# Kernel tuning notes

Measured on AMD Instinct MI355X. Metric: run time of the kernel, lower is better.

## Reference

```python
import jax, jax.numpy as jnp
import numpy as np

B, T, D, F, E, K = 2, 2048, 1024, 4096, 8, 2

def setup_inputs() -> dict:
    key = jax.random.key(0)
    k0, k1, k2, k3 = jax.random.split(key, 4)
    return {
        "x": jax.random.normal(k0, (B, T, D), jnp.float32),
        "Wg": jax.random.normal(k1, (D, E), jnp.float32) * (D ** -0.5),
        "W1": jax.random.normal(k2, (E, D, F), jnp.float32) * (D ** -0.5),
        "b1": jnp.zeros((E, F), jnp.float32),
        "W2": jax.random.normal(k3, (E, F, D), jnp.float32) * (F ** -0.5),
        "b2": jnp.zeros((E, D), jnp.float32),
        "topk": K,
    }

def reference(x, Wg, W1, b1, W2, b2, topk):
    n_experts = Wg.shape[-1]
    # Gating logits [B, T, E]
    gating = jnp.einsum('btd,de->bte', x, Wg)
    _, idx = jax.lax.top_k(gating, topk)
    # 0/1 mask of selected experts per token [B, T, E]
    mask = jax.nn.one_hot(idx, n_experts, dtype=x.dtype).sum(axis=-2)
    # Source does `gating -= 1/mask - 1`: no-op where mask==1, -inf where mask==0
    gate = jax.nn.softmax(jnp.where(mask > 0, gating, -jnp.inf), axis=-1)
    # Dense masked per-expert compute, exactly as the source (expert(x * mask_e))
    xm = x[:, :, None, :] * mask[:, :, :, None]          # [B, T, E, D]
    h = jax.nn.gelu(jnp.einsum('bted,edf->btef', xm, W1) + b1)  # [B, T, E, F]
    out_e = jnp.einsum('btef,efd->bted', h, W2) + b2     # [B, T, E, D]
    # Gate and sum over experts
    return jnp.sum(out_e * gate[..., None], axis=-2)      # [B, T, D]
```

## Files before the change

### kernel.cpp

```cpp
#include <hip/hip_runtime.h>
#include <hip/hip_bf16.h>
#include <math.h>

#define NB 2
#define NT 2048
#define NTOK 4096
#define DD 1024
#define FF 4096
#define NE 8
#define KSEL 2
#define BM 128
#define BN 128
#define BK 32
#define ROWCAP 9216
#define ROWTILES 72
#define KP2 2

typedef __attribute__((ext_vector_type(8))) short short8_t;
typedef __attribute__((ext_vector_type(4))) float f32x4;

__device__ __forceinline__ unsigned short f2bf(float f){
  unsigned u = __float_as_uint(f);
  unsigned r = (u + 0x7fffu + ((u >> 16) & 1u)) >> 16;
  return (unsigned short)r;
}

__device__ __forceinline__ int xcd_swz(int lin, int nwg){
  int q = nwg >> 3, r = nwg & 7;
  int xcd = lin & 7, idx = lin >> 3;
  return (xcd < r ? xcd * (q + 1) : r * (q + 1) + (xcd - r) * q) + idx;
}

#define GLOAD_LDS(g, l) \
  __builtin_amdgcn_global_load_lds((const __attribute__((address_space(1))) void*)(g), \
                                   (__attribute__((address_space(3))) void*)(l), 16, 0, 0)
#define VMCNT0 asm volatile("s_waitcnt vmcnt(0)" ::: "memory")
#define RAWBAR __builtin_amdgcn_s_barrier()


__global__ void k_prep(const float* __restrict__ x, const float* __restrict__ wg,
                       short* __restrict__ xb, int* __restrict__ topk_idx,
                       float* __restrict__ topk_gate, int* __restrict__ counts){
  int wid = threadIdx.x >> 6, lane = threadIdx.x & 63;
  int t = blockIdx.x * 4 + wid;
  const float* xr = x + (size_t)t * DD;
  short* xbr = xb + (size_t)t * DD;
  double acc[NE];
#pragma unroll
  for (int e = 0; e < NE; ++e) acc[e] = 0.0;
#pragma unroll
  for (int p = 0; p < 4; ++p){
    int d = p * 256 + lane * 4;
    float4 v = *(const float4*)(xr + d);
    short4 o;
    o.x = (short)f2bf(v.x); o.y = (short)f2bf(v.y);
    o.z = (short)f2bf(v.z); o.w = (short)f2bf(v.w);
    *(short4*)(xbr + d) = o;
    const float* w0 = wg + (size_t)d * NE;
    float vv[4] = {v.x, v.y, v.z, v.w};
#pragma unroll
    for (int j = 0; j < 4; ++j){
      double xv = (double)vv[j];
#pragma unroll
      for (int e = 0; e < NE; ++e) acc[e] += xv * (double)w0[j * NE + e];
    }
  }
#pragma unroll
  for (int e = 0; e < NE; ++e){
#pragma unroll
    for (int s = 32; s; s >>= 1) acc[e] += __shfl_xor(acc[e], s, 64);
  }
  if (lane == 0){
    int i0 = 0; double v0 = acc[0];
#pragma unroll
    for (int e = 1; e < NE; ++e) if (acc[e] > v0){ v0 = acc[e]; i0 = e; }
    int i1 = -1; double v1 = -1e300;
#pragma unroll
    for (int e = 0; e < NE; ++e) if (e != i0 && acc[e] > v1){ v1 = acc[e]; i1 = e; }
    double g0 = 1.0 / (1.0 + exp(v1 - v0));
    topk_idx[2 * t] = i0; topk_idx[2 * t + 1] = i1;
    topk_gate[2 * t] = (float)g0; topk_gate[2 * t + 1] = (float)(1.0 - g0);
    atomicAdd(&counts[i0], 1);
    atomicAdd(&counts[i1], 1);
  }
}


#define TS_SW(c) (4 * (((c) >> 2) & 7))

__global__ void k_transpose2(const float* __restrict__ W1, const float* __restrict__ W2,
                             short* __restrict__ w1t, short* __restrict__ w2t){
  __shared__ short T[128 * 264];
  int id = blockIdx.x;
  bool isw2 = id >= 1024;
  int rem = id & 1023;
  int e = rem >> 7, t7 = rem & 127;
  int R, C, r0, c0;
  const float* in; short* out;
  if (!isw2){ R = DD; C = FF; r0 = (t7 >> 5) * 256; c0 = (t7 & 31) * 128;
              in = W1 + (size_t)e * R * C; out = w1t + (size_t)e * R * C; }
  else      { R = FF; C = DD; r0 = (t7 >> 3) * 256; c0 = (t7 & 7) * 128;
              in = W2 + (size_t)e * R * C; out = w2t + (size_t)e * R * C; }
  int t = threadIdx.x;
  int li = t & 31, rg = t >> 5;
#pragma unroll
  for (int it = 0; it < 16; ++it){
    int r = it * 16 + rg;
    float4 v = *(const float4*)(in + (size_t)(r0 + r) * C + c0 + 4 * li);
    float vv[4] = {v.x, v.y, v.z, v.w};
#pragma unroll
    for (int j = 0; j < 4; ++j){
      int c = 4 * li + j;
      int w = (r >> 1) ^ TS_SW(c);
      T[c * 264 + w * 2 + (r & 1)] = (short)f2bf(vv[j]);
    }
  }
  __syncthreads();
#pragma unroll
  for (int it = 0; it < 8; ++it){
    int c = it * 16 + rg;
    int w0 = (4 * li) ^ TS_SW(c);
    short8_t v = *(const short8_t*)(T + c * 264 + w0 * 2);
    *(short8_t*)(out + (size_t)(c0 + c) * R + r0 + 8 * li) = v;
  }
}


__global__ void k_route_all(const int* __restrict__ counts, const int* __restrict__ topk_idx,
                            const float* __restrict__ topk_gate, int* __restrict__ poff_g,
                            int* __restrict__ row_token, float* __restrict__ row_gate,
                            int* __restrict__ slot_of){
  __shared__ int poff[NE + 1], cur[NE], rends[NE];
  if (threadIdx.x == 0){
    int off = 0;
    for (int e = 0; e < NE; ++e){
      poff[e] = off; cur[e] = off; rends[e] = off + counts[e];
      off += (counts[e] + BM - 1) & ~(BM - 1);
    }
    poff[NE] = off;
    for (int e = 0; e <= NE; ++e) poff_g[e] = poff[e];
  }
  __syncthreads();
  for (int t = threadIdx.x; t < NTOK; t += 256){
#pragma unroll
    for (int k = 0; k < KSEL; ++k){
      int e = topk_idx[2 * t + k];
      float g = topk_gate[2 * t + k];
      int slot = atomicAdd(&cur[e], 1);
      row_token[slot] = t;
      row_gate[slot] = g;
      slot_of[2 * t + k] = slot;
    }
  }
  __syncthreads();
#pragma unroll
  for (int e = 0; e < NE; ++e)
    for (int s = rends[e] + (int)threadIdx.x; s < poff[e + 1]; s += 256){
      row_token[s] = 0; row_gate[s] = 0.f;
    }
}


__launch_bounds__(256, 4)
__global__ void k_gemm1(const short* __restrict__ xb, const short* __restrict__ w1t,
                        const float* __restrict__ b1, short* __restrict__ h,
                        const int* __restrict__ row_token, const int* __restrict__ poff){
  __shared__ short As[2][BM * BK];
  __shared__ short Bs[2][BN * BK];
  int wg = xcd_swz(blockIdx.x, ROWTILES * (FF / BN));
  int g = wg >> 6, t6 = wg & 63;
  int bx = (g >> 2) * 8 + (t6 & 7);
  int by = (g & 3) * 8 + (t6 >> 3);
  int row0 = bx * BM;
  if (row0 >= poff[NE]) return;
  int e = 0;
  while (row0 >= poff[e + 1]) ++e;
  int n0 = by * BN;
  int tid = threadIdx.x;

  const short* asrc[2]; const short* bsrc[2];
#pragma unroll
  for (int p = 0; p < 2; ++p){
    int L = p * 256 + tid;
    int r = L >> 2, c = L & 3;
    int cd = c ^ ((r >> 1) & 3);
    int tok = row_token[row0 + r];
    asrc[p] = xb + (size_t)tok * DD + cd * 8;
    bsrc[p] = w1t + (size_t)e * FF * DD + (size_t)(n0 + r) * DD + cd * 8;
  }

  f32x4 acc[4][4];
#pragma unroll
  for (int i = 0; i < 4; ++i)
#pragma unroll
    for (int j = 0; j < 4; ++j) acc[i][j] = (f32x4){0.f, 0.f, 0.f, 0.f};

  int wid = tid >> 6, lane = tid & 63;
  int wr = wid >> 1, wc = wid & 1;
  int lrow = lane & 15, lk = lane >> 4;

  auto STAGE = [&](int nb, int k0){
#pragma unroll
    for (int p = 0; p < 2; ++p){
      GLOAD_LDS(asrc[p] + k0, &As[nb][0] + tid * 8 + p * 2048);
      GLOAD_LDS(bsrc[p] + k0, &Bs[nb][0] + tid * 8 + p * 2048);
    }
  };

  STAGE(0, 0);
  VMCNT0; RAWBAR;

  const int NKT = DD / BK;
#pragma unroll 1
  for (int kt = 0; kt < NKT; ++kt){
    int b = kt & 1;
    bool more = (kt + 1 < NKT);
    if (more) STAGE(b ^ 1, (kt + 1) * BK);
    short8_t a[4], bb[4];
#pragma unroll
    for (int m = 0; m < 4; ++m){
      int r = wr * 64 + m * 16 + lrow;
      a[m] = *(const short8_t*)(&As[b][0] + r * BK + ((lk ^ ((r >> 1) & 3)) * 8));
    }
#pragma unroll
    for (int n = 0; n < 4; ++n){
      int r = wc * 64 + n * 16 + lrow;
      bb[n] = *(const short8_t*)(&Bs[b][0] + r * BK + ((lk ^ ((r >> 1) & 3)) * 8));
    }
#pragma unroll
    for (int m = 0; m < 4; ++m)
#pragma unroll
      for (int n = 0; n < 4; ++n)
        acc[m][n] = __builtin_amdgcn_mfma_f32_16x16x32_bf16(a[m], bb[n], acc[m][n], 0, 0, 0);
    if (more) VMCNT0;
    RAWBAR;
  }

  const float* b1e = b1 + (size_t)e * FF;
  float bias[4];
#pragma unroll
  for (int n = 0; n < 4; ++n) bias[n] = b1e[n0 + wc * 64 + n * 16 + lrow];
#pragma unroll
  for (int m = 0; m < 4; ++m){
#pragma unroll
    for (int j = 0; j < 4; ++j){
      int row = row0 + wr * 64 + m * 16 + lk * 4 + j;
      short* hr = h + (size_t)row * FF + n0 + wc * 64 + lrow;
#pragma unroll
      for (int n = 0; n < 4; ++n){
        float v = acc[m][n][j] + bias[n];
        float u = 0.7978845608028654f * (v + 0.044715f * v * v * v);
        float gl = v / (1.0f + __expf(-2.0f * u));
        hr[n * 16] = (short)f2bf(gl);
      }
    }
  }
}


__launch_bounds__(256, 4)
__global__ void k_gemm2(const short* __restrict__ h, const short* __restrict__ w2t,
                        const float* __restrict__ b2, float* __restrict__ ya,
                        float* __restrict__ yb, const int* __restrict__ poff){
  __shared__ short As[2][BM * BK];
  __shared__ short Bs[2][BN * BK];
  int wg = xcd_swz(blockIdx.x, ROWTILES * (DD / BN) * KP2);
  int kz = wg / (ROWTILES * (DD / BN));
  int c5 = wg % (ROWTILES * (DD / BN));
  int g = c5 >> 5, t5 = c5 & 31;
  int bx = g * 4 + (t5 & 3);
  int by = t5 >> 2;
  int row0 = bx * BM;
  if (row0 >= poff[NE]) return;
  int e = 0;
  while (row0 >= poff[e + 1]) ++e;
  int n0 = by * BN;
  int tid = threadIdx.x;

  const short* asrc[2]; const short* bsrc[2];
#pragma unroll
  for (int p = 0; p < 2; ++p){
    int L = p * 256 + tid;
    int r = L >> 2, c = L & 3;
    int cd = c ^ ((r >> 1) & 3);
    asrc[p] = h + (size_t)(row0 + r) * FF + cd * 8;
    bsrc[p] = w2t + (size_t)e * DD * FF + (size_t)(n0 + r) * FF + cd * 8;
  }

  f32x4 acc[4][4];
#pragma unroll
  for (int i = 0; i < 4; ++i)
#pragma unroll
    for (int j = 0; j < 4; ++j) acc[i][j] = (f32x4){0.f, 0.f, 0.f, 0.f};

  int wid = tid >> 6, lane = tid & 63;
  int wr = wid >> 1, wc = wid & 1;
  int lrow = lane & 15, lk = lane >> 4;

  auto STAGE = [&](int nb, int k0){
#pragma unroll
    for (int p = 0; p < 2; ++p){
      GLOAD_LDS(asrc[p] + k0, &As[nb][0] + tid * 8 + p * 2048);
      GLOAD_LDS(bsrc[p] + k0, &Bs[nb][0] + tid * 8 + p * 2048);
    }
  };

  int kbeg = kz * (FF / KP2);
  STAGE(0, kbeg);
  VMCNT0; RAWBAR;

  const int NKT = (FF / KP2) / BK;
#pragma unroll 1
  for (int kt = 0; kt < NKT; ++kt){
    int b = kt & 1;
    bool more = (kt + 1 < NKT);
    if (more) STAGE(b ^ 1, kbeg + (kt + 1) * BK);
    short8_t a[4], bb[4];
#pragma unroll
    for (int m = 0; m < 4; ++m){
      int r = wr * 64 + m * 16 + lrow;
      a[m] = *(const short8_t*)(&As[b][0] + r * BK + ((lk ^ ((r >> 1) & 3)) * 8));
    }
#pragma unroll
    for (int n = 0; n < 4; ++n){
      int r = wc * 64 + n * 16 + lrow;
      bb[n] = *(const short8_t*)(&Bs[b][0] + r * BK + ((lk ^ ((r >> 1) & 3)) * 8));
    }
#pragma unroll
    for (int m = 0; m < 4; ++m)
#pragma unroll
      for (int n = 0; n < 4; ++n)
        acc[m][n] = __builtin_amdgcn_mfma_f32_16x16x32_bf16(a[m], bb[n], acc[m][n], 0, 0, 0);
    if (more) VMCNT0;
    RAWBAR;
  }

  float* y = (kz == 0) ? ya : yb;
  const float* b2e = b2 + (size_t)e * DD;
  float bias[4];
#pragma unroll
  for (int n = 0; n < 4; ++n) bias[n] = (kz == 0) ? b2e[n0 + wc * 64 + n * 16 + lrow] : 0.0f;
#pragma unroll
  for (int m = 0; m < 4; ++m){
#pragma unroll
    for (int j = 0; j < 4; ++j){
      int row = row0 + wr * 64 + m * 16 + lk * 4 + j;
      float* yr = y + (size_t)row * DD + n0 + wc * 64 + lrow;
#pragma unroll
      for (int n = 0; n < 4; ++n)
        yr[n * 16] = acc[m][n][j] + bias[n];
    }
  }
}


__global__ void k_combine(const float* __restrict__ ya, const float* __restrict__ yb,
                          const int* __restrict__ slot_of, const float* __restrict__ topk_gate,
                          float* __restrict__ out){
  int i = blockIdx.x * 256 + threadIdx.x;
  int t = i >> 8;
  int c4 = (i & 255) * 4;
  int s0 = slot_of[2 * t], s1 = slot_of[2 * t + 1];
  float g0 = topk_gate[2 * t], g1 = topk_gate[2 * t + 1];
  float4 a0 = *(const float4*)(ya + (size_t)s0 * DD + c4);
  float4 b0 = *(const float4*)(yb + (size_t)s0 * DD + c4);
  float4 a1 = *(const float4*)(ya + (size_t)s1 * DD + c4);
  float4 b1 = *(const float4*)(yb + (size_t)s1 * DD + c4);
  float4 o;
  o.x = g0 * (a0.x + b0.x) + g1 * (a1.x + b1.x);
  o.y = g0 * (a0.y + b0.y) + g1 * (a1.y + b1.y);
  o.z = g0 * (a0.z + b0.z) + g1 * (a1.z + b1.z);
  o.w = g0 * (a0.w + b0.w) + g1 * (a1.w + b1.w);
  *(float4*)(out + (size_t)t * DD + c4) = o;
}


extern "C" void kernel_launch(void* const* d_in, const int* in_sizes, int n_in,
                              void* d_out, int out_size, void* d_ws, size_t ws_size,
                              hipStream_t stream){
  (void)in_sizes; (void)n_in; (void)out_size; (void)ws_size;
  const float* x  = (const float*)d_in[0];
  const float* Wg = (const float*)d_in[1];
  const float* W1 = (const float*)d_in[2];
  const float* b1 = (const float*)d_in[3];
  const float* W2 = (const float*)d_in[4];
  const float* b2 = (const float*)d_in[5];
  float* out = (float*)d_out;
  char* ws = (char*)d_ws;

  int*   counts    = (int*)(ws + 0);
  int*   poff      = (int*)(ws + 256);
  int*   topk_idx  = (int*)(ws + 1024);
  float* topk_gate = (float*)(ws + 33792);
  int*   row_token = (int*)(ws + 66560);
  float* row_gate  = (float*)(ws + 103424);
  int*   slot_of   = (int*)(ws + 140288);
  short* xb        = (short*)(ws + 173056);
  short* w1t       = (short*)(ws + 8561664);
  short* w2t       = (short*)(ws + 75670528);
  short* h         = (short*)(ws + 142779392);
  float* ya        = (float*)(ws + 173056);
  float* yb        = (float*)(ws + 37921792);

  hipMemsetAsync(counts, 0, 32, stream);

  k_prep<<<dim3(NTOK / 4), 256, 0, stream>>>(x, Wg, xb, topk_idx, topk_gate, counts);
  k_transpose2<<<dim3(2048), 512, 0, stream>>>(W1, W2, w1t, w2t);
  k_route_all<<<dim3(1), 256, 0, stream>>>(counts, topk_idx, topk_gate, poff,
                                           row_token, row_gate, slot_of);
  k_gemm1<<<dim3(ROWTILES * (FF / BN)), 256, 0, stream>>>(xb, w1t, b1, h, row_token, poff);
  k_gemm2<<<dim3(ROWTILES * (DD / BN) * KP2), 256, 0, stream>>>(h, w2t, b2, ya, yb, poff);
  k_combine<<<dim3(NTOK * DD / 4 / 256), 256, 0, stream>>>(ya, yb, slot_of, topk_gate, out);
}
```

Measured before the change: 430.4 us.

## Load A operand directly from global into registers, dropping LDS staging for A

Both expert GEMM kernels stop staging the activation (A) tile through shared memory. Each wave instead loads its own MFMA A fragments straight from global memory into double-buffered registers, prefetching the next k-step, and only the weight tile still goes through LDS. This cuts LDS traffic and footprint, but each A row is now read from global once per column-wave instead of once per block, which raises global/L2 traffic and register pressure; occupancy hints drop from 4 to 3 and the loop is unrolled by 2.

```diff
diff --git a/kernel.cpp b/kernel.cpp
--- a/kernel.cpp
+++ b/kernel.cpp
@@ -161,11 +161,10 @@
 }
 
 
-__launch_bounds__(256, 4)
+__launch_bounds__(256, 3)
 __global__ void k_gemm1(const short* __restrict__ xb, const short* __restrict__ w1t,
                         const float* __restrict__ b1, short* __restrict__ h,
                         const int* __restrict__ row_token, const int* __restrict__ poff){
-  __shared__ short As[2][BM * BK];
   __shared__ short Bs[2][BN * BK];
   int wg = xcd_swz(blockIdx.x, ROWTILES * (FF / BN));
   int g = wg >> 6, t6 = wg & 63;
@@ -177,17 +176,25 @@
   while (row0 >= poff[e + 1]) ++e;
   int n0 = by * BN;
   int tid = threadIdx.x;
-
-  const short* asrc[2]; const short* bsrc[2];
+  int wid = tid >> 6, lane = tid & 63;
+  int wr = wid >> 1, wc = wid & 1;
+  int lrow = lane & 15, lk = lane >> 4;
+
+  const short* bsrc[2];
 #pragma unroll
   for (int p = 0; p < 2; ++p){
     int L = p * 256 + tid;
     int r = L >> 2, c = L & 3;
     int cd = c ^ ((r >> 1) & 3);
-    int tok = row_token[row0 + r];
-    asrc[p] = xb + (size_t)tok * DD + cd * 8;
     bsrc[p] = w1t + (size_t)e * FF * DD + (size_t)(n0 + r) * DD + cd * 8;
   }
+  const short* aptr[4];
+#pragma unroll
+  for (int m = 0; m < 4; ++m){
+    int r = row0 + wr * 64 + m * 16 + lrow;
+    int tok = row_token[r];
+    aptr[m] = xb + (size_t)tok * DD + lk * 8;
+  }
 
   f32x4 acc[4][4];
 #pragma unroll
@@ -195,33 +202,31 @@
 #pragma unroll
     for (int j = 0; j < 4; ++j) acc[i][j] = (f32x4){0.f, 0.f, 0.f, 0.f};
 
-  int wid = tid >> 6, lane = tid & 63;
-  int wr = wid >> 1, wc = wid & 1;
-  int lrow = lane & 15, lk = lane >> 4;
-
   auto STAGE = [&](int nb, int k0){
 #pragma unroll
-    for (int p = 0; p < 2; ++p){
-      GLOAD_LDS(asrc[p] + k0, &As[nb][0] + tid * 8 + p * 2048);
+    for (int p = 0; p < 2; ++p)
       GLOAD_LDS(bsrc[p] + k0, &Bs[nb][0] + tid * 8 + p * 2048);
-    }
   };
 
+  short8_t aA[4], aB[4];
+#pragma unroll
+  for (int m = 0; m < 4; ++m) aA[m] = *(const short8_t*)(aptr[m]);
   STAGE(0, 0);
   VMCNT0; RAWBAR;
 
   const int NKT = DD / BK;
-#pragma unroll 1
+#pragma unroll 2
   for (int kt = 0; kt < NKT; ++kt){
     int b = kt & 1;
     bool more = (kt + 1 < NKT);
-    if (more) STAGE(b ^ 1, (kt + 1) * BK);
-    short8_t a[4], bb[4];
-#pragma unroll
-    for (int m = 0; m < 4; ++m){
-      int r = wr * 64 + m * 16 + lrow;
-      a[m] = *(const short8_t*)(&As[b][0] + r * BK + ((lk ^ ((r >> 1) & 3)) * 8));
-    }
+    short8_t* acur = (kt & 1) ? aB : aA;
+    short8_t* anxt = (kt & 1) ? aA : aB;
+    if (more){
+      STAGE(b ^ 1, (kt + 1) * BK);
+#pragma unroll
+      for (int m = 0; m < 4; ++m) anxt[m] = *(const short8_t*)(aptr[m] + (kt + 1) * BK);
+    }
+    short8_t bb[4];
 #pragma unroll
     for (int n = 0; n < 4; ++n){
       int r = wc * 64 + n * 16 + lrow;
@@ -231,7 +236,7 @@
     for (int m = 0; m < 4; ++m)
 #pragma unroll
       for (int n = 0; n < 4; ++n)
-        acc[m][n] = __builtin_amdgcn_mfma_f32_16x16x32_bf16(a[m], bb[n], acc[m][n], 0, 0, 0);
+        acc[m][n] = __builtin_amdgcn_mfma_f32_16x16x32_bf16(acur[m], bb[n], acc[m][n], 0, 0, 0);
     if (more) VMCNT0;
     RAWBAR;
   }
@@ -258,11 +263,10 @@
 }
 
 
-__launch_bounds__(256, 4)
+__launch_bounds__(256, 3)
 __global__ void k_gemm2(const short* __restrict__ h, const short* __restrict__ w2t,
                         const float* __restrict__ b2, float* __restrict__ ya,
                         float* __restrict__ yb, const int* __restrict__ poff){
-  __shared__ short As[2][BM * BK];
   __shared__ short Bs[2][BN * BK];
   int wg = xcd_swz(blockIdx.x, ROWTILES * (DD / BN) * KP2);
   int kz = wg / (ROWTILES * (DD / BN));
@@ -276,15 +280,24 @@
   while (row0 >= poff[e + 1]) ++e;
   int n0 = by * BN;
   int tid = threadIdx.x;
-
-  const short* asrc[2]; const short* bsrc[2];
+  int wid = tid >> 6, lane = tid & 63;
+  int wr = wid >> 1, wc = wid & 1;
+  int lrow = lane & 15, lk = lane >> 4;
+  int kbeg = kz * (FF / KP2);
+
+  const short* bsrc[2];
 #pragma unroll
   for (int p = 0; p < 2; ++p){
     int L = p * 256 + tid;
     int r = L >> 2, c = L & 3;
     int cd = c ^ ((r >> 1) & 3);
-    asrc[p] = h + (size_t)(row0 + r) * FF + cd * 8;
-    bsrc[p] = w2t + (size_t)e * DD * FF + (size_t)(n0 + r) * FF + cd * 8;
+    bsrc[p] = w2t + (size_t)e * DD * FF + (size_t)(n0 + r) * FF + kbeg + cd * 8;
+  }
+  const short* aptr[4];
+#pragma unroll
+  for (int m = 0; m < 4; ++m){
+    int r = row0 + wr * 64 + m * 16 + lrow;
+    aptr[m] = h + (size_t)r * FF + kbeg + lk * 8;
   }
 
   f32x4 acc[4][4];
@@ -293,34 +306,31 @@
 #pragma unroll
     for (int j = 0; j < 4; ++j) acc[i][j] = (f32x4){0.f, 0.f, 0.f, 0.f};
 
-  int wid = tid >> 6, lane = tid & 63;
-  int wr = wid >> 1, wc = wid & 1;
-  int lrow = lane & 15, lk = lane >> 4;
-
   auto STAGE = [&](int nb, int k0){
 #pragma unroll
-    for (int p = 0; p < 2; ++p){
-      GLOAD_LDS(asrc[p] + k0, &As[nb][0] + tid * 8 + p * 2048);
+    for (int p = 0; p < 2; ++p)
       GLOAD_LDS(bsrc[p] + k0, &Bs[nb][0] + tid * 8 + p * 2048);
-    }
   };
 
-  int kbeg = kz * (FF / KP2);
-  STAGE(0, kbeg);
+  short8_t aA[4], aB[4];
+#pragma unroll
+  for (int m = 0; m < 4; ++m) aA[m] = *(const short8_t*)(aptr[m]);
+  STAGE(0, 0);
   VMCNT0; RAWBAR;
 
   const int NKT = (FF / KP2) / BK;
-#pragma unroll 1
+#pragma unroll 2
   for (int kt = 0; kt < NKT; ++kt){
     int b = kt & 1;
     bool more = (kt + 1 < NKT);
-    if (more) STAGE(b ^ 1, kbeg + (kt + 1) * BK);
-    short8_t a[4], bb[4];
-#pragma unroll
-    for (int m = 0; m < 4; ++m){
-      int r = wr * 64 + m * 16 + lrow;
-      a[m] = *(const short8_t*)(&As[b][0] + r * BK + ((lk ^ ((r >> 1) & 3)) * 8));
-    }
+    short8_t* acur = (kt & 1) ? aB : aA;
+    short8_t* anxt = (kt & 1) ? aA : aB;
+    if (more){
+      STAGE(b ^ 1, (kt + 1) * BK);
+#pragma unroll
+      for (int m = 0; m < 4; ++m) anxt[m] = *(const short8_t*)(aptr[m] + (kt + 1) * BK);
+    }
+    short8_t bb[4];
 #pragma unroll
     for (int n = 0; n < 4; ++n){
       int r = wc * 64 + n * 16 + lrow;
@@ -330,7 +340,7 @@
     for (int m = 0; m < 4; ++m)
 #pragma unroll
       for (int n = 0; n < 4; ++n)
-        acc[m][n] = __builtin_amdgcn_mfma_f32_16x16x32_bf16(a[m], bb[n], acc[m][n], 0, 0, 0);
+        acc[m][n] = __builtin_amdgcn_mfma_f32_16x16x32_bf16(acur[m], bb[n], acc[m][n], 0, 0, 0);
     if (more) VMCNT0;
     RAWBAR;
   }
```

Result: slower. 560.7 us (+30.3%).

## Fuse weight transpose and bf16 cast into GEMM B-tile loading

Applied to the files above, without the earlier changes.

Removes the separate kernel that transposed and converted W1/W2 to bf16. Each GEMM now loads fp32 weight tiles straight into registers, packs pairs of k values into bf16 words and writes them to a padded LDS layout that the MFMA operand reads use. This drops a full read and write pass over both weight tensors. In exchange, each row-tile block re-reads fp32 weights (twice the bytes), repeats the conversion, and does register-staged LDS stores with scalar 32-bit reads instead of async direct-to-LDS loads. It also switches to round-half-up bf16 rounding.

```diff
diff --git a/kernel.cpp b/kernel.cpp
--- a/kernel.cpp
+++ b/kernel.cpp
@@ -15,6 +15,7 @@
 #define ROWCAP 9216
 #define ROWTILES 72
 #define KP2 2
+#define BSTR 34
 
 typedef __attribute__((ext_vector_type(8))) short short8_t;
 typedef __attribute__((ext_vector_type(4))) float f32x4;
@@ -25,6 +26,10 @@
   return (unsigned short)r;
 }
 
+__device__ __forceinline__ unsigned pk2(float a, float b){
+  return ((__float_as_uint(a) + 0x8000u) >> 16) | ((__float_as_uint(b) + 0x8000u) & 0xffff0000u);
+}
+
 __device__ __forceinline__ int xcd_swz(int lin, int nwg){
   int q = nwg >> 3, r = nwg & 7;
   int xcd = lin & 7, idx = lin >> 3;
@@ -35,6 +40,7 @@
   __builtin_amdgcn_global_load_lds((const __attribute__((address_space(1))) void*)(g), \
                                    (__attribute__((address_space(3))) void*)(l), 16, 0, 0)
 #define VMCNT0 asm volatile("s_waitcnt vmcnt(0)" ::: "memory")
+#define LGKM0  asm volatile("s_waitcnt lgkmcnt(0)" ::: "memory")
 #define RAWBAR __builtin_amdgcn_s_barrier()
 
 
@@ -82,46 +88,6 @@
     topk_gate[2 * t] = (float)g0; topk_gate[2 * t + 1] = (float)(1.0 - g0);
     atomicAdd(&counts[i0], 1);
     atomicAdd(&counts[i1], 1);
-  }
-}
-
-
-#define TS_SW(c) (4 * (((c) >> 2) & 7))
-
-__global__ void k_transpose2(const float* __restrict__ W1, const float* __restrict__ W2,
-                             short* __restrict__ w1t, short* __restrict__ w2t){
-  __shared__ short T[128 * 264];
-  int id = blockIdx.x;
-  bool isw2 = id >= 1024;
-  int rem = id & 1023;
-  int e = rem >> 7, t7 = rem & 127;
-  int R, C, r0, c0;
-  const float* in; short* out;
-  if (!isw2){ R = DD; C = FF; r0 = (t7 >> 5) * 256; c0 = (t7 & 31) * 128;
-              in = W1 + (size_t)e * R * C; out = w1t + (size_t)e * R * C; }
-  else      { R = FF; C = DD; r0 = (t7 >> 3) * 256; c0 = (t7 & 7) * 128;
-              in = W2 + (size_t)e * R * C; out = w2t + (size_t)e * R * C; }
-  int t = threadIdx.x;
-  int li = t & 31, rg = t >> 5;
-#pragma unroll
-  for (int it = 0; it < 16; ++it){
-    int r = it * 16 + rg;
-    float4 v = *(const float4*)(in + (size_t)(r0 + r) * C + c0 + 4 * li);
-    float vv[4] = {v.x, v.y, v.z, v.w};
-#pragma unroll
-    for (int j = 0; j < 4; ++j){
-      int c = 4 * li + j;
-      int w = (r >> 1) ^ TS_SW(c);
-      T[c * 264 + w * 2 + (r & 1)] = (short)f2bf(vv[j]);
-    }
-  }
-  __syncthreads();
-#pragma unroll
-  for (int it = 0; it < 8; ++it){
-    int c = it * 16 + rg;
-    int w0 = (4 * li) ^ TS_SW(c);
-    short8_t v = *(const short8_t*)(T + c * 264 + w0 * 2);
-    *(short8_t*)(out + (size_t)(c0 + c) * R + r0 + 8 * li) = v;
   }
 }
 
@@ -162,11 +128,11 @@
 
 
 __launch_bounds__(256, 4)
-__global__ void k_gemm1(const short* __restrict__ xb, const short* __restrict__ w1t,
+__global__ void k_gemm1(const short* __restrict__ xb, const float* __restrict__ W1,
                         const float* __restrict__ b1, short* __restrict__ h,
                         const int* __restrict__ row_token, const int* __restrict__ poff){
   __shared__ short As[2][BM * BK];
-  __shared__ short Bs[2][BN * BK];
+  __shared__ short Bs[2][BN * BSTR];
   int wg = xcd_swz(blockIdx.x, ROWTILES * (FF / BN));
   int g = wg >> 6, t6 = wg & 63;
   int bx = (g >> 2) * 8 + (t6 & 7);
@@ -178,7 +144,7 @@
   int n0 = by * BN;
   int tid = threadIdx.x;
 
-  const short* asrc[2]; const short* bsrc[2];
+  const short* asrc[2];
 #pragma unroll
   for (int p = 0; p < 2; ++p){
     int L = p * 256 + tid;
@@ -186,8 +152,9 @@
     int cd = c ^ ((r >> 1) & 3);
     int tok = row_token[row0 + r];
     asrc[p] = xb + (size_t)tok * DD + cd * 8;
-    bsrc[p] = w1t + (size_t)e * FF * DD + (size_t)(n0 + r) * DD + cd * 8;
-  }
+  }
+  int nc = tid & 15, kp = tid >> 4;
+  const float* bsrcf = W1 + (size_t)e * DD * FF + (size_t)(2 * kp) * FF + n0 + nc * 8;
 
   f32x4 acc[4][4];
 #pragma unroll
@@ -199,41 +166,66 @@
   int wr = wid >> 1, wc = wid & 1;
   int lrow = lane & 15, lk = lane >> 4;
 
-  auto STAGE = [&](int nb, int k0){
-#pragma unroll
-    for (int p = 0; p < 2; ++p){
+  auto STAGE_A = [&](int nb, int k0){
+#pragma unroll
+    for (int p = 0; p < 2; ++p)
       GLOAD_LDS(asrc[p] + k0, &As[nb][0] + tid * 8 + p * 2048);
-      GLOAD_LDS(bsrc[p] + k0, &Bs[nb][0] + tid * 8 + p * 2048);
-    }
-  };
-
-  STAGE(0, 0);
-  VMCNT0; RAWBAR;
+  };
+  float4 rb0, rb1, rb2, rb3;
+  auto LOADB = [&](int k0){
+    const float* s = bsrcf + (size_t)k0 * FF;
+    rb0 = *(const float4*)(s);
+    rb1 = *(const float4*)(s + 4);
+    rb2 = *(const float4*)(s + FF);
+    rb3 = *(const float4*)(s + FF + 4);
+  };
+  auto PACKW = [&](int nb){
+    int* Bw = (int*)(&Bs[nb][0]);
+    int n8 = nc * 8;
+    Bw[(n8 + 0) * 17 + kp] = pk2(rb0.x, rb2.x);
+    Bw[(n8 + 1) * 17 + kp] = pk2(rb0.y, rb2.y);
+    Bw[(n8 + 2) * 17 + kp] = pk2(rb0.z, rb2.z);
+    Bw[(n8 + 3) * 17 + kp] = pk2(rb0.w, rb2.w);
+    Bw[(n8 + 4) * 17 + kp] = pk2(rb1.x, rb3.x);
+    Bw[(n8 + 5) * 17 + kp] = pk2(rb1.y, rb3.y);
+    Bw[(n8 + 6) * 17 + kp] = pk2(rb1.z, rb3.z);
+    Bw[(n8 + 7) * 17 + kp] = pk2(rb1.w, rb3.w);
+  };
+
+  LOADB(0);
+  STAGE_A(0, 0);
+  VMCNT0;
+  PACKW(0);
+  LGKM0; RAWBAR;
 
   const int NKT = DD / BK;
 #pragma unroll 1
   for (int kt = 0; kt < NKT; ++kt){
     int b = kt & 1;
     bool more = (kt + 1 < NKT);
-    if (more) STAGE(b ^ 1, (kt + 1) * BK);
+    if (more){ LOADB((kt + 1) * BK); STAGE_A(b ^ 1, (kt + 1) * BK); }
     short8_t a[4], bb[4];
 #pragma unroll
     for (int m = 0; m < 4; ++m){
       int r = wr * 64 + m * 16 + lrow;
       a[m] = *(const short8_t*)(&As[b][0] + r * BK + ((lk ^ ((r >> 1) & 3)) * 8));
     }
+    const int* Bi = (const int*)(&Bs[b][0]);
 #pragma unroll
     for (int n = 0; n < 4; ++n){
-      int r = wc * 64 + n * 16 + lrow;
-      bb[n] = *(const short8_t*)(&Bs[b][0] + r * BK + ((lk ^ ((r >> 1) & 3)) * 8));
+      int rn = wc * 64 + n * 16 + lrow;
+      int bi = rn * 17 + lk * 4;
+      int4 w4;
+      w4.x = Bi[bi]; w4.y = Bi[bi + 1]; w4.z = Bi[bi + 2]; w4.w = Bi[bi + 3];
+      bb[n] = *(short8_t*)&w4;
     }
 #pragma unroll
     for (int m = 0; m < 4; ++m)
 #pragma unroll
       for (int n = 0; n < 4; ++n)
         acc[m][n] = __builtin_amdgcn_mfma_f32_16x16x32_bf16(a[m], bb[n], acc[m][n], 0, 0, 0);
-    if (more) VMCNT0;
-    RAWBAR;
+    if (more){ VMCNT0; PACKW(b ^ 1); }
+    LGKM0; RAWBAR;
   }
 
   const float* b1e = b1 + (size_t)e * FF;
@@ -259,11 +251,11 @@
 
 
 __launch_bounds__(256, 4)
-__global__ void k_gemm2(const short* __restrict__ h, const short* __restrict__ w2t,
+__global__ void k_gemm2(const short* __restrict__ h, const float* __restrict__ W2,
                         const float* __restrict__ b2, float* __restrict__ ya,
                         float* __restrict__ yb, const int* __restrict__ poff){
   __shared__ short As[2][BM * BK];
-  __shared__ short Bs[2][BN * BK];
+  __shared__ short Bs[2][BN * BSTR];
   int wg = xcd_swz(blockIdx.x, ROWTILES * (DD / BN) * KP2);
   int kz = wg / (ROWTILES * (DD / BN));
   int c5 = wg % (ROWTILES * (DD / BN));
@@ -276,16 +268,18 @@
   while (row0 >= poff[e + 1]) ++e;
   int n0 = by * BN;
   int tid = threadIdx.x;
-
-  const short* asrc[2]; const short* bsrc[2];
+  int kbeg = kz * (FF / KP2);
+
+  const short* asrc[2];
 #pragma unroll
   for (int p = 0; p < 2; ++p){
     int L = p * 256 + tid;
     int r = L >> 2, c = L & 3;
     int cd = c ^ ((r >> 1) & 3);
-    asrc[p] = h + (size_t)(row0 + r) * FF + cd * 8;
-    bsrc[p] = w2t + (size_t)e * DD * FF + (size_t)(n0 + r) * FF + cd * 8;
-  }
+    asrc[p] = h + (size_t)(row0 + r) * FF + kbeg + cd * 8;
+  }
+  int nc = tid & 15, kp = tid >> 4;
+  const float* bsrcf = W2 + (size_t)e * FF * DD + (size_t)(kbeg + 2 * kp) * DD + n0 + nc * 8;
 
   f32x4 acc[4][4];
 #pragma unroll
@@ -297,42 +291,66 @@
   int wr = wid >> 1, wc = wid & 1;
   int lrow = lane & 15, lk = lane >> 4;
 
-  auto STAGE = [&](int nb, int k0){
-#pragma unroll
-    for (int p = 0; p < 2; ++p){
+  auto STAGE_A = [&](int nb, int k0){
+#pragma unroll
+    for (int p = 0; p < 2; ++p)
       GLOAD_LDS(asrc[p] + k0, &As[nb][0] + tid * 8 + p * 2048);
-      GLOAD_LDS(bsrc[p] + k0, &Bs[nb][0] + tid * 8 + p * 2048);
-    }
-  };
-
-  int kbeg = kz * (FF / KP2);
-  STAGE(0, kbeg);
-  VMCNT0; RAWBAR;
+  };
+  float4 rb0, rb1, rb2, rb3;
+  auto LOADB = [&](int k0){
+    const float* s = bsrcf + (size_t)k0 * DD;
+    rb0 = *(const float4*)(s);
+    rb1 = *(const float4*)(s + 4);
+    rb2 = *(const float4*)(s + DD);
+    rb3 = *(const float4*)(s + DD + 4);
+  };
+  auto PACKW = [&](int nb){
+    int* Bw = (int*)(&Bs[nb][0]);
+    int n8 = nc * 8;
+    Bw[(n8 + 0) * 17 + kp] = pk2(rb0.x, rb2.x);
+    Bw[(n8 + 1) * 17 + kp] = pk2(rb0.y, rb2.y);
+    Bw[(n8 + 2) * 17 + kp] = pk2(rb0.z, rb2.z);
+    Bw[(n8 + 3) * 17 + kp] = pk2(rb0.w, rb2.w);
+    Bw[(n8 + 4) * 17 + kp] = pk2(rb1.x, rb3.x);
+    Bw[(n8 + 5) * 17 + kp] = pk2(rb1.y, rb3.y);
+    Bw[(n8 + 6) * 17 + kp] = pk2(rb1.z, rb3.z);
+    Bw[(n8 + 7) * 17 + kp] = pk2(rb1.w, rb3.w);
+  };
+
+  LOADB(0);
+  STAGE_A(0, 0);
+  VMCNT0;
+  PACKW(0);
+  LGKM0; RAWBAR;
 
   const int NKT = (FF / KP2) / BK;
 #pragma unroll 1
   for (int kt = 0; kt < NKT; ++kt){
     int b = kt & 1;
     bool more = (kt + 1 < NKT);
-    if (more) STAGE(b ^ 1, kbeg + (kt + 1) * BK);
+    if (more){ LOADB((kt + 1) * BK); STAGE_A(b ^ 1, (kt + 1) * BK); }
     short8_t a[4], bb[4];
 #pragma unroll
     for (int m = 0; m < 4; ++m){
       int r = wr * 64 + m * 16 + lrow;
       a[m] = *(const short8_t*)(&As[b][0] + r * BK + ((lk ^ ((r >> 1) & 3)) * 8));
     }
+    const int* Bi = (const int*)(&Bs[b][0]);
 #pragma unroll
     for (int n = 0; n < 4; ++n){
-      int r = wc * 64 + n * 16 + lrow;
-      bb[n] = *(const short8_t*)(&Bs[b][0] + r * BK + ((lk ^ ((r >> 1) & 3)) * 8));
+      int rn = wc * 64 + n * 16 + lrow;
+      int bi = rn * 17 + lk * 4;
+      int4 w4;
+      w4.x = Bi[bi]; w4.y = Bi[bi + 1]; w4.z = Bi[bi + 2]; w4.w = Bi[bi + 3];
+      bb[n] = *(short8_t*)&w4;
     }
 #pragma unroll
     for (int m = 0; m < 4; ++m)
 #pragma unroll
       for (int n = 0; n < 4; ++n)
         acc[m][n] = __builtin_amdgcn_mfma_f32_16x16x32_bf16(a[m], bb[n], acc[m][n], 0, 0, 0);
-    if (more) VMCNT0;
-    RAWBAR;
+    if (more){ VMCNT0; PACKW(b ^ 1); }
+    LGKM0; RAWBAR;
   }
 
   float* y = (kz == 0) ? ya : yb;
@@ -396,8 +414,6 @@
   float* row_gate  = (float*)(ws + 103424);
   int*   slot_of   = (int*)(ws + 140288);
   short* xb        = (short*)(ws + 173056);
-  short* w1t       = (short*)(ws + 8561664);
-  short* w2t       = (short*)(ws + 75670528);
   short* h         = (short*)(ws + 142779392);
   float* ya        = (float*)(ws + 173056);
   float* yb        = (float*)(ws + 37921792);
@@ -405,10 +421,9 @@
   hipMemsetAsync(counts, 0, 32, stream);
 
   k_prep<<<dim3(NTOK / 4), 256, 0, stream>>>(x, Wg, xb, topk_idx, topk_gate, counts);
-  k_transpose2<<<dim3(2048), 512, 0, stream>>>(W1, W2, w1t, w2t);
   k_route_all<<<dim3(1), 256, 0, stream>>>(counts, topk_idx, topk_gate, poff,
                                            row_token, row_gate, slot_of);
-  k_gemm1<<<dim3(ROWTILES * (FF / BN)), 256, 0, stream>>>(xb, w1t, b1, h, row_token, poff);
-  k_gemm2<<<dim3(ROWTILES * (DD / BN) * KP2), 256, 0, stream>>>(h, w2t, b2, ya, yb, poff);
+  k_gemm1<<<dim3(ROWTILES * (FF / BN)), 256, 0, stream>>>(xb, W1, b1, h, row_token, poff);
+  k_gemm2<<<dim3(ROWTILES * (DD / BN) * KP2), 256, 0, stream>>>(h, W2, b2, ya, yb, poff);
   k_combine<<<dim3(NTOK * DD / 4 / 256), 256, 0, stream>>>(ya, yb, slot_of, topk_gate, out);
 }
```

Measured after the change: 454.7 us. +5.6%, slower.
